# Performance work log

Measured on AMD Instinct MI355X. Metric: run time of the kernel, lower is better.

Reference implementation:

```python
import jax, jax.numpy as jnp
import numpy as np

V, E, HD, K = 100000, 128, 256, 9
B, T = 128, 512
H = HD // 2  # per-direction hidden size


def setup_inputs() -> dict:
    key = jax.random.key(0)
    ks = jax.random.split(key, 16)
    s = 0.1
    rn = lambda k, shape: jax.random.normal(k, shape, jnp.float32) * s
    sentences = jax.random.randint(ks[0], (B, T), 0, V, dtype=jnp.int32)
    lengths = jax.random.randint(ks[1], (B,), 1, T + 1, dtype=jnp.int32)
    return {
        'sentences': sentences,
        'lengths': lengths,
        'embed': rn(ks[2], (V, E)),
        'Wih_f': rn(ks[3], (4 * H, E)), 'Whh_f': rn(ks[4], (4 * H, H)),
        'bih_f': rn(ks[5], (4 * H,)), 'bhh_f': rn(ks[6], (4 * H,)),
        'Wih_b': rn(ks[7], (4 * H, E)), 'Whh_b': rn(ks[8], (4 * H, H)),
        'bih_b': rn(ks[9], (4 * H,)), 'bhh_b': rn(ks[10], (4 * H,)),
        'W_out': rn(ks[11], (K, HD)), 'b_out': rn(ks[12], (K,)),
        'start_t': rn(ks[13], (K,)), 'end_t': rn(ks[14], (K,)),
        'trans': rn(ks[15], (K, K)),
    }


def _lstm(x, mask, Wih, Whh, bih, bhh, reverse):
    # x: [B,T,E], mask: [B,T] bool. Replicates packed-sequence semantics:
    # state frozen and output zeroed at padding positions (padding is trailing,
    # so reverse=True starts fresh at each sequence's true end).
    Bv, Hv = x.shape[0], Whh.shape[1]
    bias = bih + bhh

    def step(carry, inp):
        h, c = carry
        x_t, m_t = inp  # [B,E], [B,1]
        gates = x_t @ Wih.T + h @ Whh.T + bias  # [B,4H]
        i, f, g, o = jnp.split(gates, 4, axis=-1)  # torch gate order i,f,g,o
        c_new = jax.nn.sigmoid(f) * c + jax.nn.sigmoid(i) * jnp.tanh(g)
        h_new = jax.nn.sigmoid(o) * jnp.tanh(c_new)
        h = jnp.where(m_t, h_new, h)
        c = jnp.where(m_t, c_new, c)
        return (h, c), h * m_t.astype(h.dtype)

    init = (jnp.zeros((Bv, Hv), x.dtype), jnp.zeros((Bv, Hv), x.dtype))
    xs = (jnp.swapaxes(x, 0, 1), jnp.swapaxes(mask, 0, 1)[..., None])
    _, hs = jax.lax.scan(step, init, xs, reverse=reverse)
    return jnp.swapaxes(hs, 0, 1)  # [B,T,H]


def _emissions(sentences, mask, embed, Wih_f, Whh_f, bih_f, bhh_f,
               Wih_b, Whh_b, bih_b, bhh_b, W_out, b_out):
    x = embed[sentences]  # [B,T,E] (dropout is identity at inference)
    hf = _lstm(x, mask, Wih_f, Whh_f, bih_f, bhh_f, reverse=False)
    hb = _lstm(x, mask, Wih_b, Whh_b, bih_b, bhh_b, reverse=True)
    h = jnp.concatenate([hf, hb], axis=-1)  # [B,T,2H]
    return jnp.einsum('btd,kd->btk', h, W_out) + b_out  # [B,T,K]


def _viterbi(em, mask, start_t, end_t, trans):
    # torchcrf-style batched Viterbi decode. em: [B,T,K], mask: [B,T] bool.
    Kv = em.shape[-1]
    ident = jnp.arange(Kv, dtype=jnp.int32)[None]  # identity backpointers for pads
    score0 = start_t[None] + em[:, 0]  # [B,K]

    def step(score, inp):
        em_t, m_t = inp  # [B,K], [B,1]
        cand = score[:, :, None] + trans[None] + em_t[:, None, :]  # [B,K_prev,K_cur]
        new_score = cand.max(axis=1)
        idx = cand.argmax(axis=1).astype(jnp.int32)  # [B,K]
        score = jnp.where(m_t, new_score, score)
        idx = jnp.where(m_t, idx, ident)
        return score, idx

    xs = (jnp.swapaxes(em[:, 1:], 0, 1), jnp.swapaxes(mask[:, 1:], 0, 1)[..., None])
    score, hist = jax.lax.scan(step, score0, xs)  # hist: [T-1,B,K]
    score = score + end_t[None]
    last_tag = jnp.argmax(score, axis=-1).astype(jnp.int32)  # [B]

    def back(tag, idx_t):
        prev = jnp.take_along_axis(idx_t, tag[:, None], axis=1)[:, 0]
        return prev, prev

    _, tags_prev = jax.lax.scan(back, last_tag, hist, reverse=True)  # [T-1,B]
    tags = jnp.swapaxes(jnp.concatenate([tags_prev, last_tag[None]], axis=0), 0, 1)
    return jnp.where(mask, tags, 0), score.max(axis=-1)


def reference(sentences, lengths, embed, Wih_f, Whh_f, bih_f, bhh_f,
              Wih_b, Whh_b, bih_b, bhh_b, W_out, b_out, start_t, end_t, trans):
    mask = jnp.arange(sentences.shape[1])[None] < lengths[:, None]  # [B,T]
    em = _emissions(sentences, mask, embed, Wih_f, Whh_f, bih_f, bhh_f,
                    Wih_b, Whh_b, bih_b, bhh_b, W_out, b_out)
    tags, _ = _viterbi(em, mask, start_t, end_t, trans)
    return tags  # [B,T] int32, padded positions set to 0
```

## Files before the change

kernel.cpp:

```cpp
#include <hip/hip_runtime.h>
#include <cmath>

#define B_  128
#define T_  512
#define E_  128
#define H_  128
#define G4  512
#define K_  9

__global__ __launch_bounds__(256, 2)
void proj_gemm(const int* __restrict__ sent, const float* __restrict__ embed,
               const float* __restrict__ Wf, const float* __restrict__ Wb,
               const float* __restrict__ bif, const float* __restrict__ bhf,
               const float* __restrict__ bib, const float* __restrict__ bhb,
               float* __restrict__ proj, int t0f, int Tc)
{
  __shared__ __align__(16) float Al[128 * 64];
  __shared__ __align__(16) float Bl[128 * 64];
  const int tid   = threadIdx.x;
  const int ntile = blockIdx.x;
  const int mtile = blockIdx.y;
  const int tpb   = Tc >> 6;
  const int b     = mtile / tpb;
  const int toff  = (mtile - b * tpb) << 6;
  const int dir   = ntile >> 3;
  const int t0    = dir ? (T_ - t0f - Tc) : t0f;
  const float* __restrict__ W = dir ? Wb : Wf;
  const int n0 = (ntile & 7) << 6;

  {
    const int r  = tid & 63;
    const int kc = tid >> 6;
    const int t  = t0 + toff + r;
    const int vid = sent[b * T_ + t];
    const float* arow = embed + (size_t)vid * E_ + kc * 32;
    const float* brow = W + (size_t)(n0 + r) * E_ + kc * 32;
#pragma unroll
    for (int q = 0; q < 8; ++q) {
      float4 av = *(const float4*)(arow + q * 4);
      float4 bv = *(const float4*)(brow + q * 4);
      int k0 = kc * 32 + q * 4;
      Al[(k0 + 0) * 64 + r] = av.x; Al[(k0 + 1) * 64 + r] = av.y;
      Al[(k0 + 2) * 64 + r] = av.z; Al[(k0 + 3) * 64 + r] = av.w;
      Bl[(k0 + 0) * 64 + r] = bv.x; Bl[(k0 + 1) * 64 + r] = bv.y;
      Bl[(k0 + 2) * 64 + r] = bv.z; Bl[(k0 + 3) * 64 + r] = bv.w;
    }
  }
  __syncthreads();

  const int mg = tid & 15, ng = tid >> 4;
  float acc[4][4] = {};
#pragma unroll 8
  for (int k = 0; k < 128; ++k) {
    float4 a  = *(const float4*)&Al[k * 64 + mg * 4];
    float4 bb = *(const float4*)&Bl[k * 64 + ng * 4];
    acc[0][0] += a.x * bb.x; acc[0][1] += a.x * bb.y; acc[0][2] += a.x * bb.z; acc[0][3] += a.x * bb.w;
    acc[1][0] += a.y * bb.x; acc[1][1] += a.y * bb.y; acc[1][2] += a.y * bb.z; acc[1][3] += a.y * bb.w;
    acc[2][0] += a.z * bb.x; acc[2][1] += a.z * bb.y; acc[2][2] += a.z * bb.z; acc[2][3] += a.z * bb.w;
    acc[3][0] += a.w * bb.x; acc[3][1] += a.w * bb.y; acc[3][2] += a.w * bb.z; acc[3][3] += a.w * bb.w;
  }

  const float* bi = dir ? bib : bif;
  const float* bh = dir ? bhb : bhf;
  const int nl = ng * 4;
  float4 bias;
  bias.x = bi[n0 + nl + 0] + bh[n0 + nl + 0];
  bias.y = bi[n0 + nl + 1] + bh[n0 + nl + 1];
  bias.z = bi[n0 + nl + 2] + bh[n0 + nl + 2];
  bias.w = bi[n0 + nl + 3] + bh[n0 + nl + 3];
#pragma unroll
  for (int i = 0; i < 4; ++i) {
    const int tloc = toff + mg * 4 + i;
    float4 o;
    o.x = acc[i][0] + bias.x; o.y = acc[i][1] + bias.y;
    o.z = acc[i][2] + bias.z; o.w = acc[i][3] + bias.w;
    *(float4*)&proj[((size_t)(b * Tc + tloc)) * 1024 + dir * G4 + n0 + nl] = o;
  }
}

__device__ __forceinline__ float fast_rcp(float x) {
  return __builtin_amdgcn_rcpf(x);
}
__device__ __forceinline__ float fast_sig(float x) {
  return fast_rcp(1.f + __expf(-x));
}
__device__ __forceinline__ float fast_tanh(float x) {
  return 2.f * fast_rcp(1.f + __expf(-2.f * x)) - 1.f;
}

__global__ __launch_bounds__(512, 2)
void lstm_chunk(const float* __restrict__ proj,
                const float* __restrict__ Whf, const float* __restrict__ Whb,
                const int* __restrict__ lengths,
                float* __restrict__ hs,
                float* __restrict__ sh, float* __restrict__ sc,
                int t0f, int Tc, int first)
{
  const int dir = blockIdx.x;
  const int b   = blockIdx.y;
  const int tid = threadIdx.x;
  const int l   = tid & 63;
  const int wv  = tid >> 6;
  const int u   = wv * 16 + (l & 15);
  const int gp  = (l >> 4) & 1;
  const int kh  = l >> 5;
  const int rowA = u + (gp ? 256 : 0);
  const int rowB = rowA + 128;
  const float* __restrict__ Whh = dir ? Whb : Whf;
  __shared__ __align__(16) float h_hist[2][H_];

  float wA[64], wB[64];
  {
    const float* wra = Whh + (size_t)rowA * H_ + kh * 64;
    const float* wrb = Whh + (size_t)rowB * H_ + kh * 64;
#pragma unroll
    for (int k = 0; k < 64; k += 4) {
      float4 va = *(const float4*)(wra + k);
      float4 vb = *(const float4*)(wrb + k);
      wA[k] = va.x; wA[k + 1] = va.y; wA[k + 2] = va.z; wA[k + 3] = va.w;
      wB[k] = vb.x; wB[k + 1] = vb.y; wB[k + 2] = vb.z; wB[k + 3] = vb.w;
    }
  }
#pragma unroll
  for (int k = 0; k < 64; ++k) {
    asm volatile("" : "+v"(wA[k]));
    asm volatile("" : "+v"(wB[k]));
  }

  const int len = lengths[b];
  const int t0  = dir ? (T_ - t0f - Tc) : t0f;
  const float fgp = (float)gp;
  const float kf  = 1.f + fgp;
  float c = 0.f, h_reg = 0.f;
  if (!first) {
    c     = sc[(dir * B_ + b) * H_ + u];
    h_reg = sh[(dir * B_ + b) * H_ + u];
  }
  if (l < 16) h_hist[1][u] = h_reg;
  __syncthreads();

  const float* projpA = proj + (size_t)b * Tc * 1024 + dir * G4 + rowA;
  const float* projpB = projpA + 128;
  const int tc00 = dir ? (Tc - 1) : 0;
  float pvA = projpA[(size_t)tc00 * 1024];
  float pvB = projpB[(size_t)tc00 * 1024];

  for (int s = 0; s < Tc; ++s) {
    const int tc = dir ? (Tc - 1 - s) : s;
    const int t  = t0 + tc;
    float nvA = 0.f, nvB = 0.f;
    if (s + 1 < Tc) {
      const int tcn = dir ? (Tc - 2 - s) : (s + 1);
      nvA = projpA[(size_t)tcn * 1024];
      nvB = projpB[(size_t)tcn * 1024];
    }
    const float* hp = h_hist[(s + 1) & 1] + kh * 64;
    float a0 = 0.f, a1 = 0.f, a2 = 0.f, a3 = 0.f;
#pragma unroll
    for (int k4 = 0; k4 < 16; ++k4) {
      float4 h4 = *(const float4*)&hp[k4 * 4];
      a0 += wA[4 * k4 + 0] * h4.x; a1 += wA[4 * k4 + 1] * h4.y;
      a0 += wA[4 * k4 + 2] * h4.z; a1 += wA[4 * k4 + 3] * h4.w;
      a2 += wB[4 * k4 + 0] * h4.x; a3 += wB[4 * k4 + 1] * h4.y;
      a2 += wB[4 * k4 + 2] * h4.z; a3 += wB[4 * k4 + 3] * h4.w;
    }
    float sA = a0 + a1; sA += __shfl_xor(sA, 32); sA += pvA;
    float sB = a2 + a3; sB += __shfl_xor(sB, 32); sB += pvB;
    const float gA = kf * fast_rcp(1.f + __expf(-kf * sA)) - fgp;
    const float gB = fast_sig(sB);
    const float xA = __shfl_xor(gA, 16);
    const float xB = __shfl_xor(gB, 16);
    const float gi = gp ? xA : gA;
    const float gf = gp ? xB : gB;
    const float gg = gp ? gA : xA;
    const float go = gp ? gB : xB;
    const float cn = gf * c + gi * gg;
    const float hn = go * fast_tanh(cn);
    const bool  m  = (t < len);
    c     = m ? cn : c;
    h_reg = m ? hn : h_reg;
    if (l < 16) {
      h_hist[s & 1][u] = h_reg;
      hs[(size_t)(b * T_ + t) * 256 + dir * H_ + u] = m ? hn : 0.f;
    }
    __syncthreads();
    pvA = nvA; pvB = nvB;
  }
  if (l < 16 && wv == (u >> 4)) {
    sh[(dir * B_ + b) * H_ + u] = h_reg;
    sc[(dir * B_ + b) * H_ + u] = c;
  }
}

__global__ __launch_bounds__(256)
void emis_kernel(const float* __restrict__ hs, const float* __restrict__ Wout,
                 const float* __restrict__ bout, float* __restrict__ em)
{
  __shared__ __align__(16) float Wl[K_ * 256];
  const int tid = threadIdx.x;
  for (int i = tid; i < K_ * 256; i += 256) Wl[i] = Wout[i];
  __syncthreads();
  const int m = blockIdx.x * 256 + tid;
  const float* h = hs + (size_t)m * 256;
  float acc[K_] = {};
#pragma unroll 4
  for (int kk = 0; kk < 64; ++kk) {
    float4 h4 = *(const float4*)(h + kk * 4);
#pragma unroll
    for (int k9 = 0; k9 < K_; ++k9) {
      float4 w4 = *(const float4*)&Wl[k9 * 256 + kk * 4];
      acc[k9] += h4.x * w4.x + h4.y * w4.y + h4.z * w4.z + h4.w * w4.w;
    }
  }
#pragma unroll
  for (int k9 = 0; k9 < K_; ++k9) em[(size_t)m * K_ + k9] = acc[k9] + bout[k9];
}

__global__ __launch_bounds__(64)
void viterbi_kernel(const float* __restrict__ em, const int* __restrict__ lengths,
                    const float* __restrict__ st, const float* __restrict__ en,
                    const float* __restrict__ trans, int* __restrict__ tags)
{
  const int b    = blockIdx.x;
  const int lane = threadIdx.x;
  __shared__ unsigned char hist[(T_ - 1) * 16];
  const int len = lengths[b];
  float tr[K_];
#pragma unroll
  for (int j = 0; j < K_; ++j) tr[j] = (lane < K_) ? trans[j * K_ + lane] : 0.f;
  float s = (lane < K_) ? st[lane] + em[(size_t)(b * T_) * K_ + lane] : -1e30f;
  for (int t = 1; t < len; ++t) {
    float best = -1e30f; int bj = 0;
#pragma unroll
    for (int j = 0; j < K_; ++j) {
      float v = __shfl(s, j) + tr[j];
      if (v > best) { best = v; bj = j; }
    }
    if (lane < K_) {
      s = best + em[(size_t)(b * T_ + t) * K_ + lane];
      hist[(t - 1) * 16 + lane] = (unsigned char)bj;
    }
  }
  float fs = (lane < K_) ? s + en[lane] : -1e30f;
  float best = -1e30f; int last = 0;
#pragma unroll
  for (int j = 0; j < K_; ++j) {
    float v = __shfl(fs, j);
    if (v > best) { best = v; last = j; }
  }
  __syncthreads();
  if (lane == 0) {
    int tag = last;
    tags[b * T_ + len - 1] = tag;
    for (int t = len - 2; t >= 0; --t) {
      tag = hist[t * 16 + tag];
      tags[b * T_ + t] = tag;
    }
  }
  for (int t = len + lane; t < T_; t += 64) tags[b * T_ + t] = 0;
}

extern "C" void kernel_launch(void* const* d_in, const int* in_sizes, int n_in,
                              void* d_out, int out_size, void* d_ws, size_t ws_size,
                              hipStream_t stream)
{
  const int*   sent  = (const int*)d_in[0];
  const int*   lens  = (const int*)d_in[1];
  const float* embed = (const float*)d_in[2];
  const float* Wif   = (const float*)d_in[3];
  const float* Whf   = (const float*)d_in[4];
  const float* bif   = (const float*)d_in[5];
  const float* bhf   = (const float*)d_in[6];
  const float* Wib   = (const float*)d_in[7];
  const float* Whb   = (const float*)d_in[8];
  const float* bib   = (const float*)d_in[9];
  const float* bhb   = (const float*)d_in[10];
  const float* Wout  = (const float*)d_in[11];
  const float* bout  = (const float*)d_in[12];
  const float* stt   = (const float*)d_in[13];
  const float* ent   = (const float*)d_in[14];
  const float* trans = (const float*)d_in[15];
  int* tags = (int*)d_out;

  float* ws   = (float*)d_ws;
  float* hs   = ws;
  float* em   = hs + (size_t)B_ * T_ * 256;
  float* sh   = em + (size_t)B_ * T_ * K_;
  float* sc   = sh + (size_t)2 * B_ * H_;
  float* proj = sc + (size_t)2 * B_ * H_;
  const size_t fixed_bytes = (size_t)(proj - ws) * sizeof(float);

  int Tc = 512;
  while (Tc > 64 && fixed_bytes + (size_t)B_ * Tc * 1024 * sizeof(float) > ws_size)
    Tc >>= 1;

  const int nch = T_ / Tc;
  for (int c2 = 0; c2 < nch; ++c2) {
    const int t0f = c2 * Tc;
    dim3 g1(16, B_ * (Tc >> 6));
    hipLaunchKernelGGL(proj_gemm, g1, dim3(256), 0, stream,
                       sent, embed, Wif, Wib, bif, bhf, bib, bhb, proj, t0f, Tc);
    dim3 g2(2, B_);
    hipLaunchKernelGGL(lstm_chunk, g2, dim3(512), 0, stream,
                       proj, Whf, Whb, lens, hs, sh, sc, t0f, Tc, (int)(c2 == 0));
  }
  hipLaunchKernelGGL(emis_kernel, dim3((B_ * T_) / 256), dim3(256), 0, stream,
                     hs, Wout, bout, em);
  hipLaunchKernelGGL(viterbi_kernel, dim3(B_), dim3(64), 0, stream,
                     em, lens, stt, ent, trans, tags);
}
```

Before: 845.8 us.

## Pre-gather embeddings and pre-transpose input weights into K-major layouts for projection GEMM

Adds a gather kernel that writes embedding rows into a K-major [E, B*T] buffer and a kernel that transposes both input-weight matrices into a K-major [E, 1024] buffer. The projection GEMM then fills shared memory with coalesced float4 loads and float4 stores instead of strided per-row gathers and scalar transposing stores. The cost is two extra launches and extra workspace traffic (a 32 MB Xt write and read), which also shrinks the workspace left for the proj buffer and may force smaller time chunks.

```diff
diff --git a/kernel.cpp b/kernel.cpp
--- a/kernel.cpp
+++ b/kernel.cpp
@@ -8,9 +8,35 @@
 #define G4  512
 #define K_  9
 
+__global__ __launch_bounds__(256)
+void gather_x(const int* __restrict__ sent, const float* __restrict__ embed,
+              float* __restrict__ Xt)
+{
+  const int m = blockIdx.x * 256 + threadIdx.x;
+  const int vid = sent[m];
+  const float* er = embed + (size_t)vid * E_;
+  const size_t MT = (size_t)B_ * T_;
+#pragma unroll
+  for (int q = 0; q < 32; ++q) {
+    float4 v = *(const float4*)(er + q * 4);
+    Xt[(size_t)(q * 4 + 0) * MT + m] = v.x;
+    Xt[(size_t)(q * 4 + 1) * MT + m] = v.y;
+    Xt[(size_t)(q * 4 + 2) * MT + m] = v.z;
+    Xt[(size_t)(q * 4 + 3) * MT + m] = v.w;
+  }
+}
+
+__global__ __launch_bounds__(256)
+void transpose_w(const float* __restrict__ Wf, const float* __restrict__ Wb,
+                 float* __restrict__ Wt)
+{
+  const int idx = blockIdx.x * 256 + threadIdx.x;
+  const int k = idx >> 10, n = idx & 1023;
+  Wt[idx] = (n < 512) ? Wf[n * E_ + k] : Wb[(n - 512) * E_ + k];
+}
+
 __global__ __launch_bounds__(256, 2)
-void proj_gemm(const int* __restrict__ sent, const float* __restrict__ embed,
-               const float* __restrict__ Wf, const float* __restrict__ Wb,
+void proj_gemm(const float* __restrict__ Xt, const float* __restrict__ Wt,
                const float* __restrict__ bif, const float* __restrict__ bhf,
                const float* __restrict__ bib, const float* __restrict__ bhb,
                float* __restrict__ proj, int t0f, int Tc)
@@ -25,25 +51,21 @@
   const int toff  = (mtile - b * tpb) << 6;
   const int dir   = ntile >> 3;
   const int t0    = dir ? (T_ - t0f - Tc) : t0f;
-  const float* __restrict__ W = dir ? Wb : Wf;
-  const int n0 = (ntile & 7) << 6;
+  const int n0    = (ntile & 7) << 6;
 
   {
-    const int r  = tid & 63;
-    const int kc = tid >> 6;
-    const int t  = t0 + toff + r;
-    const int vid = sent[b * T_ + t];
-    const float* arow = embed + (size_t)vid * E_ + kc * 32;
-    const float* brow = W + (size_t)(n0 + r) * E_ + kc * 32;
-#pragma unroll
-    for (int q = 0; q < 8; ++q) {
-      float4 av = *(const float4*)(arow + q * 4);
-      float4 bv = *(const float4*)(brow + q * 4);
-      int k0 = kc * 32 + q * 4;
-      Al[(k0 + 0) * 64 + r] = av.x; Al[(k0 + 1) * 64 + r] = av.y;
-      Al[(k0 + 2) * 64 + r] = av.z; Al[(k0 + 3) * 64 + r] = av.w;
-      Bl[(k0 + 0) * 64 + r] = bv.x; Bl[(k0 + 1) * 64 + r] = bv.y;
-      Bl[(k0 + 2) * 64 + r] = bv.z; Bl[(k0 + 3) * 64 + r] = bv.w;
+    const int r4 = tid & 15;
+    const int ks = tid >> 4;
+    const size_t MT = (size_t)B_ * T_;
+    const int mbase = b * T_ + t0 + toff;
+    const int nbase = dir * 512 + n0;
+#pragma unroll
+    for (int p = 0; p < 8; ++p) {
+      const int k = ks * 8 + p;
+      float4 a4 = *(const float4*)(Xt + (size_t)k * MT + mbase + r4 * 4);
+      float4 b4 = *(const float4*)(Wt + k * 1024 + nbase + r4 * 4);
+      *(float4*)&Al[k * 64 + r4 * 4] = a4;
+      *(float4*)&Bl[k * 64 + r4 * 4] = b4;
     }
   }
   __syncthreads();
@@ -287,19 +309,26 @@
   float* em   = hs + (size_t)B_ * T_ * 256;
   float* sh   = em + (size_t)B_ * T_ * K_;
   float* sc   = sh + (size_t)2 * B_ * H_;
-  float* proj = sc + (size_t)2 * B_ * H_;
+  float* Xt   = sc + (size_t)2 * B_ * H_;
+  float* Wt   = Xt + (size_t)E_ * B_ * T_;
+  float* proj = Wt + (size_t)E_ * 1024;
   const size_t fixed_bytes = (size_t)(proj - ws) * sizeof(float);
 
   int Tc = 512;
   while (Tc > 64 && fixed_bytes + (size_t)B_ * Tc * 1024 * sizeof(float) > ws_size)
     Tc >>= 1;
+
+  hipLaunchKernelGGL(gather_x, dim3((B_ * T_) / 256), dim3(256), 0, stream,
+                     sent, embed, Xt);
+  hipLaunchKernelGGL(transpose_w, dim3((E_ * 1024) / 256), dim3(256), 0, stream,
+                     Wif, Wib, Wt);
 
   const int nch = T_ / Tc;
   for (int c2 = 0; c2 < nch; ++c2) {
     const int t0f = c2 * Tc;
     dim3 g1(16, B_ * (Tc >> 6));
     hipLaunchKernelGGL(proj_gemm, g1, dim3(256), 0, stream,
-                       sent, embed, Wif, Wib, bif, bhf, bib, bhb, proj, t0f, Tc);
+                       Xt, Wt, bif, bhf, bib, bhb, proj, t0f, Tc);
     dim3 g2(2, B_);
     hipLaunchKernelGGL(lstm_chunk, g2, dim3(512), 0, stream,
                        proj, Whf, Whb, lens, hs, sh, sc, t0f, Tc, (int)(c2 == 0));
```

After: 850.9 us. Within noise of the previous version (+0.6%).
